# Kernel optimization log

Hardware: AMD Instinct MI355X
Metric: run time of the kernel (lower is better)

Reference implementation:

```python
import jax, jax.numpy as jnp
import numpy as np
import math

FREQ_SEL = [(0, 0), (0, 1), (1, 0), (1, 1)]


def _dct_mat(N):
    # Faithful replica of the module's custom dct1d matrix:
    # A[i, j] = cos(pi * j * (2i + 1) / (2N)) * sqrt(2/N), with row 0 scaled by sqrt(0.5).
    i = np.arange(N, dtype=np.float32)[:, None]
    j = np.arange(N, dtype=np.float32)[None, :]
    A = np.cos(math.pi * j * (2.0 * i + 1.0) / (2.0 * N)) * math.sqrt(2.0 / N)
    A[0] *= math.sqrt(0.5)
    return jnp.asarray(A, dtype=jnp.float32)


def _basis(H, W):
    # coeff(u, v) = sum_{h,w} A_H[u, h] * A_W[v, w] * x[h, w]
    # (both DCT stages in the torch code contract against ROWS of A)
    A_H = _dct_mat(H)
    A_W = _dct_mat(W)
    planes = [A_H[u][:, None] * A_W[v][None, :] for (u, v) in FREQ_SEL]
    return jnp.stack(planes, axis=0)  # [F, H, W]


def setup_inputs() -> dict:
    key = jax.random.key(0)
    k1, k2, k3 = jax.random.split(key, 3)
    B, C, H, W = 32, 256, 64, 64
    hidden = C // 4
    x = jax.random.normal(k1, (B, C, H, W), dtype=jnp.float32)
    w1 = jax.random.normal(k2, (hidden, C), dtype=jnp.float32) * (1.0 / math.sqrt(C))
    w2 = jax.random.normal(k3, (C, hidden), dtype=jnp.float32) * (1.0 / math.sqrt(hidden))
    return {"x": x, "w1": w1, "w2": w2}


def reference(x, w1, w2):
    B, C, H, W = x.shape
    basis = _basis(H, W)                      # [F, H, W]
    spectral = jnp.einsum('bchw,fhw->bcf', x, basis)   # [B, C, F]
    y = jnp.einsum('bcf,hc->bhf', spectral, w1)        # fc1 (1x1 conv1d)
    y = jax.nn.relu(y)
    y = jnp.einsum('bhf,ch->bcf', y, w2)               # fc2
    gate = jax.nn.sigmoid(jnp.mean(y, axis=-1))        # [B, C]
    return x * gate[:, :, None, None]
```

## Files before the change

kernel.cpp:

```cpp
#include <hip/hip_runtime.h>

#define B_  32
#define C_  256
#define HID 64
#define HW  4096
#define F_  4
#define CHUNK_B 16

typedef float fvec4 __attribute__((ext_vector_type(4)));

__global__ __launch_bounds__(256) void spectral_kernel(
        const float* __restrict__ x, float* __restrict__ spectral, int b0) {
    const int plane = b0 * C_ + blockIdx.x;
    const int t = threadIdx.x;

    __shared__ float r0[64], r1[64];
    if (t < 64) {
        float fh = (float)t;
        r0[t] = cosf(fh * 0.02454369260617026f) * 0.125f;
        r1[t] = cosf(fh * 0.07363107781851077f) * 0.17677669529663689f;
    }
    __syncthreads();

    const fvec4* xv = (const fvec4*)x + (size_t)plane * (HW / 4);
    float f0 = 0.f, f1 = 0.f, f2 = 0.f, f3 = 0.f;

    #pragma unroll
    for (int q = 0; q < 4; ++q) {
        int v = q * 256 + t;
        fvec4 d = xv[v];
        int h  = v >> 4;
        int wb = (v & 15) << 2;
        float r0h = r0[h], r1h = r1[h];
        float e, t0, t1;
        e = d.x; t0 = e * r0[wb+0]; t1 = e * r1[wb+0];
        f0 += r0h*t0; f1 += r0h*t1; f2 += r1h*t0; f3 += r1h*t1;
        e = d.y; t0 = e * r0[wb+1]; t1 = e * r1[wb+1];
        f0 += r0h*t0; f1 += r0h*t1; f2 += r1h*t0; f3 += r1h*t1;
        e = d.z; t0 = e * r0[wb+2]; t1 = e * r1[wb+2];
        f0 += r0h*t0; f1 += r0h*t1; f2 += r1h*t0; f3 += r1h*t1;
        e = d.w; t0 = e * r0[wb+3]; t1 = e * r1[wb+3];
        f0 += r0h*t0; f1 += r0h*t1; f2 += r1h*t0; f3 += r1h*t1;
    }

    #pragma unroll
    for (int off = 32; off >= 1; off >>= 1) {
        f0 += __shfl_down(f0, off);
        f1 += __shfl_down(f1, off);
        f2 += __shfl_down(f2, off);
        f3 += __shfl_down(f3, off);
    }
    __shared__ float part[4][F_];
    int wave = t >> 6, lane = t & 63;
    if (lane == 0) { part[wave][0]=f0; part[wave][1]=f1; part[wave][2]=f2; part[wave][3]=f3; }
    __syncthreads();
    if (t == 0) {
        fvec4 s;
        s.x = part[0][0]+part[1][0]+part[2][0]+part[3][0];
        s.y = part[0][1]+part[1][1]+part[2][1]+part[3][1];
        s.z = part[0][2]+part[1][2]+part[2][2]+part[3][2];
        s.w = part[0][3]+part[1][3]+part[2][3]+part[3][3];
        ((fvec4*)spectral)[plane] = s;
    }
}

__global__ __launch_bounds__(256) void gate_kernel(
        const float* __restrict__ spectral, const float* __restrict__ w1,
        const float* __restrict__ w2, float* __restrict__ gate, int b0) {
    const int b = b0 + blockIdx.x;
    const int t = threadIdx.x;

    __shared__ float s[C_][F_];
    __shared__ float y[HID][F_];

    ((fvec4*)&s[0][0])[t] = ((const fvec4*)(spectral + (size_t)b * C_ * F_))[t];
    __syncthreads();

    {
        int h = t >> 2, f = t & 3;
        const float* w1r = w1 + h * C_;
        float a0 = 0.f, a1 = 0.f, a2 = 0.f, a3 = 0.f;
        #pragma unroll 4
        for (int c = 0; c < C_; c += 4) {
            a0 += s[c+0][f] * w1r[c+0];
            a1 += s[c+1][f] * w1r[c+1];
            a2 += s[c+2][f] * w1r[c+2];
            a3 += s[c+3][f] * w1r[c+3];
        }
        y[h][f] = fmaxf((a0 + a1) + (a2 + a3), 0.f);
    }
    __syncthreads();

    {
        const float* w2r = w2 + t * HID;
        float a0=0.f, a1=0.f, a2=0.f, a3=0.f;
        #pragma unroll 8
        for (int h = 0; h < HID; ++h) {
            float wv = w2r[h];
            a0 += y[h][0]*wv; a1 += y[h][1]*wv; a2 += y[h][2]*wv; a3 += y[h][3]*wv;
        }
        float m = (a0 + a1 + a2 + a3) * 0.25f;
        gate[b * C_ + t] = 1.f / (1.f + __expf(-m));
    }
}

__global__ __launch_bounds__(256) void scale_kernel(
        const float* __restrict__ x, const float* __restrict__ gate,
        float* __restrict__ out, long long start4, long long n4) {
    long long i = start4 + (long long)blockIdx.x * 256 + threadIdx.x;
    const long long end = start4 + n4;
    const long long stride = (long long)gridDim.x * 256;
    for (; i < end; i += stride) {
        fvec4 v = ((const fvec4*)x)[i];
        float g = gate[i >> 10];
        v *= g;
        __builtin_nontemporal_store(v, ((fvec4*)out) + i);
    }
}

extern "C" void kernel_launch(void* const* d_in, const int* in_sizes, int n_in,
                              void* d_out, int out_size, void* d_ws, size_t ws_size,
                              hipStream_t stream) {
    const float* x  = (const float*)d_in[0];
    const float* w1 = (const float*)d_in[1];
    const float* w2 = (const float*)d_in[2];
    float* out = (float*)d_out;

    float* spectral = (float*)d_ws;
    float* gate     = (float*)d_ws + (size_t)B_ * C_ * F_;

    const long long chunk4 = (long long)CHUNK_B * C_ * HW / 4;

    for (int chunk = 0; chunk < B_ / CHUNK_B; ++chunk) {
        const int b0 = chunk * CHUNK_B;
        spectral_kernel<<<CHUNK_B * C_, 256, 0, stream>>>(x, spectral, b0);
        gate_kernel<<<CHUNK_B, 256, 0, stream>>>(spectral, w1, w2, gate, b0);
        scale_kernel<<<2048, 256, 0, stream>>>(x, gate, out,
                                               (long long)b0 * C_ * HW / 4, chunk4);
    }
}
```

Baseline: 84.24 us.

## Fuse gate MLP into scale kernel and drop batch chunking

Merges the gate computation and the scaling pass into one kernel in which each block recomputes the fc1 MLP for its batch item and then scales four channels. It also removes the two-chunk loop, so only two launches are made instead of six. This removes the serial low-parallelism gate kernel (16 blocks) and the launch gaps between stages. In exchange, fc1 is recomputed redundantly in every block (64 times per batch item), and x is no longer reused from L2 within a chunk because spectral now covers the full 128MB before scaling starts.

```diff
diff --git a/kernel.cpp b/kernel.cpp
--- a/kernel.cpp
+++ b/kernel.cpp
@@ -5,13 +5,12 @@
 #define HID 64
 #define HW  4096
 #define F_  4
-#define CHUNK_B 16
 
 typedef float fvec4 __attribute__((ext_vector_type(4)));
 
 __global__ __launch_bounds__(256) void spectral_kernel(
-        const float* __restrict__ x, float* __restrict__ spectral, int b0) {
-    const int plane = b0 * C_ + blockIdx.x;
+        const float* __restrict__ x, float* __restrict__ spectral) {
+    const int plane = blockIdx.x;
     const int t = threadIdx.x;
 
     __shared__ float r0[64], r1[64];
@@ -64,16 +63,20 @@
     }
 }
 
-__global__ __launch_bounds__(256) void gate_kernel(
-        const float* __restrict__ spectral, const float* __restrict__ w1,
-        const float* __restrict__ w2, float* __restrict__ gate, int b0) {
-    const int b = b0 + blockIdx.x;
-    const int t = threadIdx.x;
+__global__ __launch_bounds__(256) void gate_scale_kernel(
+        const float* __restrict__ x, const float* __restrict__ spectral,
+        const float* __restrict__ w1, const float* __restrict__ w2,
+        float* __restrict__ out) {
+    const int j  = blockIdx.x;
+    const int b  = j >> 6;
+    const int c0 = (j & 63) << 2;
+    const int t  = threadIdx.x;
 
     __shared__ float s[C_][F_];
     __shared__ float y[HID][F_];
+    __shared__ float g4[4];
 
-    ((fvec4*)&s[0][0])[t] = ((const fvec4*)(spectral + (size_t)b * C_ * F_))[t];
+    ((fvec4*)&s[0][0])[t] = ((const fvec4*)spectral)[b * C_ + t];
     __syncthreads();
 
     {
@@ -92,29 +95,24 @@
     __syncthreads();
 
     {
-        const float* w2r = w2 + t * HID;
-        float a0=0.f, a1=0.f, a2=0.f, a3=0.f;
-        #pragma unroll 8
-        for (int h = 0; h < HID; ++h) {
-            float wv = w2r[h];
-            a0 += y[h][0]*wv; a1 += y[h][1]*wv; a2 += y[h][2]*wv; a3 += y[h][3]*wv;
-        }
-        float m = (a0 + a1 + a2 + a3) * 0.25f;
-        gate[b * C_ + t] = 1.f / (1.f + __expf(-m));
+        int wv = t >> 6, lane = t & 63;
+        int c = c0 + wv;
+        float v = w2[c * HID + lane] *
+                  (0.25f * ((y[lane][0] + y[lane][1]) + (y[lane][2] + y[lane][3])));
+        #pragma unroll
+        for (int off = 32; off >= 1; off >>= 1) v += __shfl_down(v, off);
+        if (lane == 0) g4[wv] = 1.f / (1.f + __expf(-v));
     }
-}
+    __syncthreads();
 
-__global__ __launch_bounds__(256) void scale_kernel(
-        const float* __restrict__ x, const float* __restrict__ gate,
-        float* __restrict__ out, long long start4, long long n4) {
-    long long i = start4 + (long long)blockIdx.x * 256 + threadIdx.x;
-    const long long end = start4 + n4;
-    const long long stride = (long long)gridDim.x * 256;
-    for (; i < end; i += stride) {
-        fvec4 v = ((const fvec4*)x)[i];
-        float g = gate[i >> 10];
-        v *= g;
-        __builtin_nontemporal_store(v, ((fvec4*)out) + i);
+    const fvec4* xv = (const fvec4*)x   + (size_t)(b * C_ + c0) * (HW / 4);
+    fvec4*       ov = (fvec4*)      out + (size_t)(b * C_ + c0) * (HW / 4);
+    #pragma unroll
+    for (int q = 0; q < 16; ++q) {
+        int i = q * 256 + t;
+        fvec4 d = xv[i];
+        d *= g4[i >> 10];
+        __builtin_nontemporal_store(d, ov + i);
     }
 }
 
@@ -127,15 +125,7 @@
     float* out = (float*)d_out;
 
     float* spectral = (float*)d_ws;
-    float* gate     = (float*)d_ws + (size_t)B_ * C_ * F_;
 
-    const long long chunk4 = (long long)CHUNK_B * C_ * HW / 4;
-
-    for (int chunk = 0; chunk < B_ / CHUNK_B; ++chunk) {
-        const int b0 = chunk * CHUNK_B;
-        spectral_kernel<<<CHUNK_B * C_, 256, 0, stream>>>(x, spectral, b0);
-        gate_kernel<<<CHUNK_B, 256, 0, stream>>>(spectral, w1, w2, gate, b0);
-        scale_kernel<<<2048, 256, 0, stream>>>(x, gate, out,
-                                               (long long)b0 * C_ * HW / 4, chunk4);
-    }
+    spectral_kernel<<<B_ * C_, 256, 0, stream>>>(x, spectral);
+    gate_scale_kernel<<<B_ * C_ / 4, 256, 0, stream>>>(x, spectral, w1, w2, out);
 }
```

Result: faster. 74.01 us (-12.1%).

## Drop batch chunking and issue four independent nontemporal loads per scale thread

Applied to the files above, without the earlier changes.

Replaces the two-chunk loop of spectral, gate and scale launches with one pass of each kernel over the full batch, cutting six launches to three. The scale kernel drops its grid-stride loop: each thread now issues four independent nontemporal loads spaced a quarter of the tensor apart, scales them by their gates and stores them nontemporally. The goal is fewer launch gaps and more memory requests in flight. The trade-off is the loss of the chunking schedule, which kept only half of x between the reduction pass and the scale pass so that the second read could hit in cache.

```diff
diff --git a/kernel.cpp b/kernel.cpp
--- a/kernel.cpp
+++ b/kernel.cpp
@@ -5,13 +5,12 @@
 #define HID 64
 #define HW  4096
 #define F_  4
-#define CHUNK_B 16
 
 typedef float fvec4 __attribute__((ext_vector_type(4)));
 
 __global__ __launch_bounds__(256) void spectral_kernel(
-        const float* __restrict__ x, float* __restrict__ spectral, int b0) {
-    const int plane = b0 * C_ + blockIdx.x;
+        const float* __restrict__ x, float* __restrict__ spectral) {
+    const int plane = blockIdx.x;
     const int t = threadIdx.x;
 
     __shared__ float r0[64], r1[64];
@@ -66,8 +65,8 @@
 
 __global__ __launch_bounds__(256) void gate_kernel(
         const float* __restrict__ spectral, const float* __restrict__ w1,
-        const float* __restrict__ w2, float* __restrict__ gate, int b0) {
-    const int b = b0 + blockIdx.x;
+        const float* __restrict__ w2, float* __restrict__ gate) {
+    const int b = blockIdx.x;
     const int t = threadIdx.x;
 
     __shared__ float s[C_][F_];
@@ -106,16 +105,30 @@
 
 __global__ __launch_bounds__(256) void scale_kernel(
         const float* __restrict__ x, const float* __restrict__ gate,
-        float* __restrict__ out, long long start4, long long n4) {
-    long long i = start4 + (long long)blockIdx.x * 256 + threadIdx.x;
-    const long long end = start4 + n4;
-    const long long stride = (long long)gridDim.x * 256;
-    for (; i < end; i += stride) {
-        fvec4 v = ((const fvec4*)x)[i];
-        float g = gate[i >> 10];
-        v *= g;
-        __builtin_nontemporal_store(v, ((fvec4*)out) + i);
-    }
+        float* __restrict__ out) {
+    const long long base = (long long)blockIdx.x * 256 + threadIdx.x;
+    const long long S = 8192LL * 256;
+    const int gi = blockIdx.x >> 2;
+
+    const fvec4* xv = (const fvec4*)x;
+    fvec4*       ov = (fvec4*)out;
+
+    fvec4 d0 = __builtin_nontemporal_load(xv + base);
+    fvec4 d1 = __builtin_nontemporal_load(xv + base + S);
+    fvec4 d2 = __builtin_nontemporal_load(xv + base + 2*S);
+    fvec4 d3 = __builtin_nontemporal_load(xv + base + 3*S);
+
+    const float g0 = gate[gi];
+    const float g1 = gate[gi + 2048];
+    const float g2 = gate[gi + 4096];
+    const float g3 = gate[gi + 6144];
+
+    d0 *= g0; d1 *= g1; d2 *= g2; d3 *= g3;
+
+    __builtin_nontemporal_store(d0, ov + base);
+    __builtin_nontemporal_store(d1, ov + base + S);
+    __builtin_nontemporal_store(d2, ov + base + 2*S);
+    __builtin_nontemporal_store(d3, ov + base + 3*S);
 }
 
 extern "C" void kernel_launch(void* const* d_in, const int* in_sizes, int n_in,
@@ -129,13 +142,7 @@
     float* spectral = (float*)d_ws;
     float* gate     = (float*)d_ws + (size_t)B_ * C_ * F_;
 
-    const long long chunk4 = (long long)CHUNK_B * C_ * HW / 4;
-
-    for (int chunk = 0; chunk < B_ / CHUNK_B; ++chunk) {
-        const int b0 = chunk * CHUNK_B;
-        spectral_kernel<<<CHUNK_B * C_, 256, 0, stream>>>(x, spectral, b0);
-        gate_kernel<<<CHUNK_B, 256, 0, stream>>>(spectral, w1, w2, gate, b0);
-        scale_kernel<<<2048, 256, 0, stream>>>(x, gate, out,
-                                               (long long)b0 * C_ * HW / 4, chunk4);
-    }
+    spectral_kernel<<<B_ * C_, 256, 0, stream>>>(x, spectral);
+    gate_kernel<<<B_, 256, 0, stream>>>(spectral, w1, w2, gate);
+    scale_kernel<<<8192, 256, 0, stream>>>(x, gate, out);
 }
```

After: 73.40 us. 12.9% less time.
